# Kernel tuning notes

Hardware: AMD Instinct MI355X
Metric: run time of the kernel (lower is better)

The kernel has to match this reference:

```python
import jax, jax.numpy as jnp
import numpy as np

HIDDEN = 2048
N_EXPERTS = 8
TOP_K = 2
MOE_INTER = 1408
NORM_TOPK = False  # config.norm_topk_prob


def setup_inputs() -> dict:
    key = jax.random.key(0)
    k0, k1, k2, k3, k4 = jax.random.split(key, 5)
    hidden_states = jax.random.normal(k0, (2, 2048, HIDDEN), dtype=jnp.float32)
    # router gate: nn.Linear(hidden, num_experts, bias=False) -> store as [H, E]
    gate_w = jax.random.normal(k1, (HIDDEN, N_EXPERTS), dtype=jnp.float32) * 0.02
    # per-expert MLP weights, stacked over experts (Linear is x @ W.T, stored pre-transposed)
    w_gate = jax.random.normal(k2, (N_EXPERTS, HIDDEN, MOE_INTER), dtype=jnp.float32) * 0.02
    w_up = jax.random.normal(k3, (N_EXPERTS, HIDDEN, MOE_INTER), dtype=jnp.float32) * 0.02
    w_down = jax.random.normal(k4, (N_EXPERTS, MOE_INTER, HIDDEN), dtype=jnp.float32) * 0.02
    return {"hidden_states": hidden_states, "gate_w": gate_w,
            "w_gate": w_gate, "w_up": w_up, "w_down": w_down}


def reference(hidden_states, gate_w, w_gate, w_up, w_down):
    B, S, H = hidden_states.shape
    x = hidden_states.reshape(-1, H)                      # [T, H]
    T = x.shape[0]
    router_logits = x @ gate_w                            # [T, E]
    probs = jax.nn.softmax(router_logits.astype(jnp.float32), axis=-1)
    routing_weights, selected = jax.lax.top_k(probs, TOP_K)  # [T, K], [T, K]
    if NORM_TOPK:
        routing_weights = routing_weights / routing_weights.sum(-1, keepdims=True)
    routing_weights = routing_weights.astype(x.dtype)
    # dense combine weights [T, E]: scatter top-k weights to expert slots
    combine = jnp.zeros((T, N_EXPERTS), dtype=x.dtype)
    combine = combine.at[jnp.arange(T)[:, None], selected].add(routing_weights)
    # run all experts densely (reference form of gather-MLP-scatter)
    g = jnp.einsum('th,ehf->tef', x, w_gate)              # [T, E, F]
    u = jnp.einsum('th,ehf->tef', x, w_up)
    h = jax.nn.silu(g) * u
    y = jnp.einsum('tef,efh->teh', h, w_down)             # [T, E, H]
    out = jnp.einsum('te,teh->th', combine, y)            # [T, H]
    return out
```

## Files before the change

kernel.cpp:

```cpp
#include <hip/hip_runtime.h>
#include <hip/hip_bf16.h>

#define HID  2048
#define NEXP 8
#define FINT 1408
#define TM   128
#define BK   32
#define GU_NP 11
#define DN_NP 8
#define MAXT 96

typedef __bf16 bf16_t;
typedef __bf16 bf16x8 __attribute__((ext_vector_type(8)));
typedef float  f32x4  __attribute__((ext_vector_type(4)));

#define AS1 __attribute__((address_space(1)))
#define AS3 __attribute__((address_space(3)))

__device__ __forceinline__ void gll16(const void* g, void* l) {
    __builtin_amdgcn_global_load_lds((const AS1 void*)g, (AS3 void*)l, 16, 0, 0);
}

#define VMCNT6() asm volatile("s_waitcnt vmcnt(6)" ::: "memory")
#define VMCNT0() asm volatile("s_waitcnt vmcnt(0)" ::: "memory")
#define SB0() __builtin_amdgcn_sched_barrier(0)

__global__ __launch_bounds__(64) void router_kernel(
    const float* __restrict__ x, const float* __restrict__ gw,
    int* __restrict__ cnt, int* __restrict__ topk_id, float* __restrict__ topk_w,
    bf16_t* __restrict__ xb, int T)
{
    int t = blockIdx.x;
    if (t >= T) return;
    int lane = threadIdx.x;
    float acc[NEXP];
#pragma unroll
    for (int e = 0; e < NEXP; ++e) acc[e] = 0.f;
    const float* xr = x + (size_t)t * HID;
    bf16_t* xo = xb + (size_t)t * HID;
    for (int i = lane; i < HID; i += 64) {
        float xv = xr[i];
        xo[i] = (bf16_t)xv;
        const float4* g4 = (const float4*)(gw + (size_t)i * NEXP);
        float4 a = g4[0], b = g4[1];
        acc[0] += xv * a.x; acc[1] += xv * a.y; acc[2] += xv * a.z; acc[3] += xv * a.w;
        acc[4] += xv * b.x; acc[5] += xv * b.y; acc[6] += xv * b.z; acc[7] += xv * b.w;
    }
#pragma unroll
    for (int d = 1; d < 64; d <<= 1) {
#pragma unroll
        for (int e = 0; e < NEXP; ++e) acc[e] += __shfl_xor(acc[e], d, 64);
    }
    float mx = acc[0];
#pragma unroll
    for (int e = 1; e < NEXP; ++e) mx = fmaxf(mx, acc[e]);
    float p[NEXP]; float s = 0.f;
#pragma unroll
    for (int e = 0; e < NEXP; ++e) { p[e] = expf(acc[e] - mx); s += p[e]; }
    float inv = 1.f / s;
    int i1 = 0;
#pragma unroll
    for (int e = 1; e < NEXP; ++e) if (acc[e] > acc[i1]) i1 = e;
    int i2 = (i1 == 0) ? 1 : 0;
#pragma unroll
    for (int e = 0; e < NEXP; ++e) if (e != i1 && acc[e] > acc[i2]) i2 = e;
    if (lane == 0) {
        topk_id[t * 2 + 0] = i1; topk_id[t * 2 + 1] = i2;
        topk_w[t * 2 + 0] = p[i1] * inv; topk_w[t * 2 + 1] = p[i2] * inv;
        atomicAdd(&cnt[i1], 1); atomicAdd(&cnt[i2], 1);
    }
}

__global__ void offsets_kernel(const int* __restrict__ cnt, int* __restrict__ offs,
                               int* __restrict__ tile_e, int* __restrict__ tile_r,
                               int* __restrict__ ntl)
{
    if (threadIdx.x == 0) {
        int s = 0;
        for (int e = 0; e < NEXP; ++e) { offs[e] = s; s += cnt[e]; }
        offs[NEXP] = s;
        int k = 0;
        for (int e = 0; e < NEXP; ++e)
            for (int rb = 0; rb < cnt[e] && k < MAXT; rb += TM) { tile_e[k] = e; tile_r[k] = rb; ++k; }
        ntl[0] = k;
    }
}

__global__ void scatter_kernel(
    const int* __restrict__ topk_id, const int* __restrict__ offs, int* __restrict__ fill,
    int* __restrict__ tok, int* __restrict__ slot_of, int T)
{
    int t = blockIdx.x * blockDim.x + threadIdx.x;
    if (t >= T) return;
#pragma unroll
    for (int k = 0; k < 2; ++k) {
        int e = topk_id[t * 2 + k];
        int pos = atomicAdd(&fill[e], 1);
        int slot = offs[e] + pos;
        tok[slot] = t;
        slot_of[t * 2 + k] = slot;
    }
}

__global__ __launch_bounds__(256) void cvt_t_kernel(
    const float* __restrict__ in, bf16_t* __restrict__ outb, int R, int C)
{
    int tilesR = R >> 6, tilesC = C >> 6;
    int per = tilesR * tilesC;
    int e = blockIdx.x / per;
    int rem = blockIdx.x - e * per;
    int tr = rem / tilesC, tc = rem - tr * tilesC;
    const float* src = in + (size_t)e * R * C + (size_t)(tr * 64) * C + tc * 64;
    bf16_t* dst = outb + (size_t)e * R * C + (size_t)(tc * 64) * R + tr * 64;

    __shared__ float tile[64][65];
    int tid = threadIdx.x;
    int rr = tid >> 4;
    int cc = (tid & 15) * 4;
#pragma unroll
    for (int i = 0; i < 4; ++i) {
        float4 v = *(const float4*)(src + (size_t)(rr + i * 16) * C + cc);
        tile[rr + i * 16][cc + 0] = v.x; tile[rr + i * 16][cc + 1] = v.y;
        tile[rr + i * 16][cc + 2] = v.z; tile[rr + i * 16][cc + 3] = v.w;
    }
    __syncthreads();
    int oc = tid >> 2;
    int og = (tid & 3) * 16;
    bf16_t* dp = dst + (size_t)oc * R + og;
    bf16x8 o0, o1;
#pragma unroll
    for (int j = 0; j < 8; ++j) { o0[j] = (bf16_t)tile[og + j][oc]; o1[j] = (bf16_t)tile[og + 8 + j][oc]; }
    *(bf16x8*)dp = o0;
    *(bf16x8*)(dp + 8) = o1;
}

__global__ __launch_bounds__(256, 2) void gateup3_kernel(
    const bf16_t* __restrict__ xb, const bf16_t* __restrict__ wgb, const bf16_t* __restrict__ wub,
    const int* __restrict__ offs, const int* __restrict__ tok,
    const int* __restrict__ tile_e, const int* __restrict__ tile_r, const int* __restrict__ ntl,
    bf16_t* __restrict__ h_buf)
{
    __shared__ bf16_t smem[36864];
    const int ntiles = ntl[0];
    const int nitems = ntiles * GU_NP;
    const int tid = threadIdx.x;
    const int lane = tid & 63, w = tid >> 6;
    const int lr = lane & 15, lg = lane >> 4;
    const int rl = lane >> 2;
    const int sw8 = ((lane & 3) ^ ((lane >> 3) & 3)) * 8;
    const int ksw = (lg ^ ((lr >> 1) & 3)) * 8;

    for (int item = blockIdx.x; item < nitems; item += (int)gridDim.x) {
        const int ti = item / GU_NP;
        const int fp = item - ti * GU_NP;
        const int e = tile_e[ti], rbase = tile_r[ti];
        const int seg0 = offs[e];
        const int nvalid = min(offs[e + 1] - seg0 - rbase, TM);
        const int row0 = seg0 + rbase;
        const int f0 = fp * 128;

        const bf16_t* aP[2];
#pragma unroll
        for (int i = 0; i < 2; ++i) {
            int r = w * 32 + i * 16 + rl;
            int tk = tok[row0 + min(r, nvalid - 1)];
            aP[i] = xb + (size_t)tk * HID + sw8;
        }
        const bf16_t* bP[4];
#pragma unroll
        for (int j = 0; j < 4; ++j) {
            int br = w * 64 + j * 16 + rl;
            const bf16_t* W = (br < 128) ? wgb : wub;
            bP[j] = W + ((size_t)e * FINT + f0 + (br & 127)) * HID + sw8;
        }

        f32x4 acc[8][4];
#pragma unroll
        for (int mi = 0; mi < 8; ++mi)
#pragma unroll
            for (int ni = 0; ni < 4; ++ni) acc[mi][ni] = (f32x4){0.f, 0.f, 0.f, 0.f};

        auto STAGE = [&](int b, int kt) {
            int k0 = kt * BK;
            bf16_t* A = smem + b * 4096;
            bf16_t* B = smem + 12288 + b * 8192;
            gll16(aP[0] + k0, A + (w * 2 + 0) * 512);
            gll16(aP[1] + k0, A + (w * 2 + 1) * 512);
            gll16(bP[0] + k0, B + (w * 4 + 0) * 512);
            gll16(bP[1] + k0, B + (w * 4 + 1) * 512);
            gll16(bP[2] + k0, B + (w * 4 + 2) * 512);
            gll16(bP[3] + k0, B + (w * 4 + 3) * 512);
        };
        auto COMPUTE = [&](int b) {
            const bf16_t* A = smem + b * 4096;
            const bf16_t* B = smem + 12288 + b * 8192;
            bf16x8 bfr[4];
#pragma unroll
            for (int ni = 0; ni < 4; ++ni)
                bfr[ni] = *(const bf16x8*)&B[(w * 64 + ni * 16 + lr) * BK + ksw];
#pragma unroll
            for (int mi = 0; mi < 8; ++mi) {
                bf16x8 a = *(const bf16x8*)&A[(mi * 16 + lr) * BK + ksw];
#pragma unroll
                for (int ni = 0; ni < 4; ++ni)
                    acc[mi][ni] = __builtin_amdgcn_mfma_f32_16x16x32_bf16(a, bfr[ni], acc[mi][ni], 0, 0, 0);
            }
        };

        const int NK = HID / BK;
        STAGE(0, 0); STAGE(1, 1);
        int c0 = 0, c1 = 1, c2 = 2;
        for (int kt = 0; kt < NK - 1; ++kt) {
            SB0(); VMCNT6(); __builtin_amdgcn_s_barrier(); SB0();
            if (kt + 2 < NK) STAGE(c2, kt + 2);
            SB0();
            COMPUTE(c0);
            int t = c0; c0 = c1; c1 = c2; c2 = t;
        }
        SB0(); VMCNT0(); __builtin_amdgcn_s_barrier(); SB0();
        COMPUTE(c0);
        __syncthreads();

        if (w >= 2) {
#pragma unroll
            for (int mi = 0; mi < 8; ++mi)
#pragma unroll
                for (int ni = 0; ni < 4; ++ni)
#pragma unroll
                    for (int rr = 0; rr < 4; ++rr) {
                        int row = mi * 16 + lg * 4 + rr;
                        int col = (w - 2) * 64 + ni * 16 + lr;
                        smem[row * 128 + col] = (bf16_t)acc[mi][ni][rr];
                    }
        }
        __syncthreads();
        if (w < 2) {
#pragma unroll
            for (int mi = 0; mi < 8; ++mi)
#pragma unroll
                for (int ni = 0; ni < 4; ++ni)
#pragma unroll
                    for (int rr = 0; rr < 4; ++rr) {
                        int row = mi * 16 + lg * 4 + rr;
                        int col = w * 64 + ni * 16 + lr;
                        float g = acc[mi][ni][rr];
                        float u = (float)smem[row * 128 + col];
                        float h = (g / (1.f + __expf(-g))) * u;
                        if (row < nvalid)
                            h_buf[(size_t)(row0 + row) * FINT + f0 + col] = (bf16_t)h;
                    }
        }
        __syncthreads();
    }
}

__global__ __launch_bounds__(256, 2) void down3_kernel(
    const bf16_t* __restrict__ h_buf, const bf16_t* __restrict__ wdb,
    const int* __restrict__ offs, const int* __restrict__ tile_e, const int* __restrict__ tile_r,
    const int* __restrict__ ntl, bf16_t* __restrict__ y_buf)
{
    __shared__ bf16_t smem[36864];
    const int ntiles = ntl[0];
    const int nitems = ntiles * DN_NP;
    const int tid = threadIdx.x;
    const int lane = tid & 63, w = tid >> 6;
    const int lr = lane & 15, lg = lane >> 4;
    const int rl = lane >> 2;
    const int sw8 = ((lane & 3) ^ ((lane >> 3) & 3)) * 8;
    const int ksw = (lg ^ ((lr >> 1) & 3)) * 8;

    for (int item = blockIdx.x; item < nitems; item += (int)gridDim.x) {
        const int ti = item / DN_NP;
        const int hp = item - ti * DN_NP;
        const int e = tile_e[ti], rbase = tile_r[ti];
        const int seg0 = offs[e];
        const int nvalid = min(offs[e + 1] - seg0 - rbase, TM);
        const int row0 = seg0 + rbase;
        const int h0 = hp * 256;

        const bf16_t* aP[2];
#pragma unroll
        for (int i = 0; i < 2; ++i) {
            int r = w * 32 + i * 16 + rl;
            aP[i] = h_buf + (size_t)(row0 + r) * FINT + sw8;
        }
        const bf16_t* bP[4];
#pragma unroll
        for (int j = 0; j < 4; ++j) {
            int br = w * 64 + j * 16 + rl;
            bP[j] = wdb + ((size_t)e * HID + h0 + br) * FINT + sw8;
        }

        f32x4 acc[8][4];
#pragma unroll
        for (int mi = 0; mi < 8; ++mi)
#pragma unroll
            for (int ni = 0; ni < 4; ++ni) acc[mi][ni] = (f32x4){0.f, 0.f, 0.f, 0.f};

        auto STAGE = [&](int b, int kt) {
            int k0 = kt * BK;
            bf16_t* A = smem + b * 4096;
            bf16_t* B = smem + 12288 + b * 8192;
            gll16(aP[0] + k0, A + (w * 2 + 0) * 512);
            gll16(aP[1] + k0, A + (w * 2 + 1) * 512);
            gll16(bP[0] + k0, B + (w * 4 + 0) * 512);
            gll16(bP[1] + k0, B + (w * 4 + 1) * 512);
            gll16(bP[2] + k0, B + (w * 4 + 2) * 512);
            gll16(bP[3] + k0, B + (w * 4 + 3) * 512);
        };
        auto COMPUTE = [&](int b) {
            const bf16_t* A = smem + b * 4096;
            const bf16_t* B = smem + 12288 + b * 8192;
            bf16x8 bfr[4];
#pragma unroll
            for (int ni = 0; ni < 4; ++ni)
                bfr[ni] = *(const bf16x8*)&B[(w * 64 + ni * 16 + lr) * BK + ksw];
#pragma unroll
            for (int mi = 0; mi < 8; ++mi) {
                bf16x8 a = *(const bf16x8*)&A[(mi * 16 + lr) * BK + ksw];
#pragma unroll
                for (int ni = 0; ni < 4; ++ni)
                    acc[mi][ni] = __builtin_amdgcn_mfma_f32_16x16x32_bf16(a, bfr[ni], acc[mi][ni], 0, 0, 0);
            }
        };

        const int NK = FINT / BK;
        STAGE(0, 0); STAGE(1, 1);
        int c0 = 0, c1 = 1, c2 = 2;
        for (int kt = 0; kt < NK - 1; ++kt) {
            SB0(); VMCNT6(); __builtin_amdgcn_s_barrier(); SB0();
            if (kt + 2 < NK) STAGE(c2, kt + 2);
            SB0();
            COMPUTE(c0);
            int t = c0; c0 = c1; c1 = c2; c2 = t;
        }
        SB0(); VMCNT0(); __builtin_amdgcn_s_barrier(); SB0();
        COMPUTE(c0);

#pragma unroll
        for (int mi = 0; mi < 8; ++mi)
#pragma unroll
            for (int ni = 0; ni < 4; ++ni)
#pragma unroll
                for (int rr = 0; rr < 4; ++rr) {
                    int row = mi * 16 + lg * 4 + rr;
                    int col = w * 64 + ni * 16 + lr;
                    if (row < nvalid)
                        y_buf[(size_t)(row0 + row) * HID + h0 + col] = (bf16_t)acc[mi][ni][rr];
                }
        __syncthreads();
    }
}

__global__ __launch_bounds__(256) void combine_kernel(
    const bf16_t* __restrict__ y, const int* __restrict__ slot_of,
    const float* __restrict__ topk_w, float* __restrict__ out, int T)
{
    int t = blockIdx.x;
    int tid = threadIdx.x;
    int s0 = slot_of[t * 2], s1 = slot_of[t * 2 + 1];
    float w0 = topk_w[t * 2], w1 = topk_w[t * 2 + 1];
    const bf16x8* y0 = (const bf16x8*)(y + (size_t)s0 * HID);
    const bf16x8* y1 = (const bf16x8*)(y + (size_t)s1 * HID);
    bf16x8 v0 = y0[tid], v1 = y1[tid];
    float* op = out + (size_t)t * HID + tid * 8;
#pragma unroll
    for (int j = 0; j < 8; ++j)
        op[j] = w0 * (float)v0[j] + w1 * (float)v1[j];
}

extern "C" void kernel_launch(void* const* d_in, const int* in_sizes, int n_in,
                              void* d_out, int out_size, void* d_ws, size_t ws_size,
                              hipStream_t stream)
{
    const float* x  = (const float*)d_in[0];
    const float* gw = (const float*)d_in[1];
    const float* wg = (const float*)d_in[2];
    const float* wu = (const float*)d_in[3];
    const float* wd = (const float*)d_in[4];
    float* out = (float*)d_out;
    int T = in_sizes[0] / HID;
    int S2 = 2 * T;

    char* base = (char*)d_ws;
    int* cnt     = (int*)base;
    int* fill    = cnt + 8;
    int* offs    = cnt + 16;
    int* ntl     = cnt + 28;
    int* tile_e  = cnt + 32;
    int* tile_r  = cnt + 128;
    int* topk_id = cnt + 224;
    float* topk_w = (float*)(topk_id + S2);
    int* tok     = (int*)(topk_w + S2);
    int* slot_of = tok + S2 + 256;
    size_t small_end = (size_t)((char*)(slot_of + S2) - base);
    size_t cur = (small_end + 255) & ~(size_t)255;
    auto take = [&](size_t bytes) -> size_t {
        size_t o = cur; cur += bytes; cur = (cur + 255) & ~(size_t)255; return o;
    };
    size_t wbytes = (size_t)NEXP * HID * FINT * 2;
    size_t o_xb  = take((size_t)T * HID * 2);
    size_t o_wgb = take(wbytes);
    size_t o_wub = take(wbytes);
    size_t o_wdb = take(wbytes);
    size_t o_h   = take((size_t)(S2 + 256) * FINT * 2);
    size_t o_y   = take((size_t)(S2 + 256) * HID * 2);
    (void)ws_size;

    bf16_t* xb   = (bf16_t*)(base + o_xb);
    bf16_t* wgb  = (bf16_t*)(base + o_wgb);
    bf16_t* wub  = (bf16_t*)(base + o_wub);
    bf16_t* wdb  = (bf16_t*)(base + o_wdb);
    bf16_t* h_buf = (bf16_t*)(base + o_h);
    bf16_t* y_buf = (bf16_t*)(base + o_y);

    hipMemsetAsync(base, 0, 64, stream);

    router_kernel<<<T, 64, 0, stream>>>(x, gw, cnt, topk_id, topk_w, xb, T);
    offsets_kernel<<<1, 64, 0, stream>>>(cnt, offs, tile_e, tile_r, ntl);
    scatter_kernel<<<(T + 255) / 256, 256, 0, stream>>>(topk_id, offs, fill, tok, slot_of, T);

    int gridW = NEXP * (HID / 64) * (FINT / 64);
    cvt_t_kernel<<<gridW, 256, 0, stream>>>(wg, wgb, HID, FINT);
    cvt_t_kernel<<<gridW, 256, 0, stream>>>(wu, wub, HID, FINT);
    cvt_t_kernel<<<gridW, 256, 0, stream>>>(wd, wdb, FINT, HID);

    gateup3_kernel<<<512, 256, 0, stream>>>(xb, wgb, wub, offs, tok, tile_e, tile_r, ntl, h_buf);
    down3_kernel<<<512, 256, 0, stream>>>(h_buf, wdb, offs, tile_e, tile_r, ntl, y_buf);
    combine_kernel<<<T, 256, 0, stream>>>(y_buf, slot_of, topk_w, out, T);
}
```

Baseline: 504.5 us.

## Use 256-row tiles with 512-thread blocks and XCD-aware weight-panel scheduling

Doubles the M tile to 256 token rows and moves the expert GEMMs to 512-thread blocks with a 4x2 wave layout, so each weight panel is loaded once for twice as many tokens. The offsets kernel now builds per-XCD work lists that group items by weight panel (expert, column panel), so blocks on the same XCD share panels in L2. It also folds the pipeline epilogue into the main loop. The cost is more LDS per block (96KB) and coarser load balance, since there are fewer, larger work items.

```diff
diff --git a/kernel.cpp b/kernel.cpp
--- a/kernel.cpp
+++ b/kernel.cpp
@@ -4,11 +4,10 @@
 #define HID  2048
 #define NEXP 8
 #define FINT 1408
-#define TM   128
+#define TM   256
 #define BK   32
-#define GU_NP 11
-#define DN_NP 8
-#define MAXT 96
+#define GU_NPAN 88
+#define DN_NPAN 64
 
 typedef __bf16 bf16_t;
 typedef __bf16 bf16x8 __attribute__((ext_vector_type(8)));
@@ -21,7 +20,7 @@
     __builtin_amdgcn_global_load_lds((const AS1 void*)g, (AS3 void*)l, 16, 0, 0);
 }
 
-#define VMCNT6() asm volatile("s_waitcnt vmcnt(6)" ::: "memory")
+#define VMCNT4() asm volatile("s_waitcnt vmcnt(4)" ::: "memory")
 #define VMCNT0() asm volatile("s_waitcnt vmcnt(0)" ::: "memory")
 #define SB0() __builtin_amdgcn_sched_barrier(0)
 
@@ -72,17 +71,34 @@
 }
 
 __global__ void offsets_kernel(const int* __restrict__ cnt, int* __restrict__ offs,
-                               int* __restrict__ tile_e, int* __restrict__ tile_r,
-                               int* __restrict__ ntl)
+                               int* __restrict__ gbase, int* __restrict__ gcount,
+                               int* __restrict__ dbase, int* __restrict__ dcount,
+                               int* __restrict__ gu, int* __restrict__ dn)
 {
     if (threadIdx.x == 0) {
         int s = 0;
         for (int e = 0; e < NEXP; ++e) { offs[e] = s; s += cnt[e]; }
         offs[NEXP] = s;
         int k = 0;
-        for (int e = 0; e < NEXP; ++e)
-            for (int rb = 0; rb < cnt[e] && k < MAXT; rb += TM) { tile_e[k] = e; tile_r[k] = rb; ++k; }
-        ntl[0] = k;
+        for (int x = 0; x < 8; ++x) {
+            gbase[x] = k;
+            for (int p = x; p < GU_NPAN; p += 8) {
+                int e = p / 11, fp = p - e * 11;
+                int nt = (cnt[e] + TM - 1) / TM;
+                for (int t = 0; t < nt; ++t) gu[k++] = (e << 10) | (fp << 6) | t;
+            }
+            gcount[x] = k - gbase[x];
+        }
+        k = 0;
+        for (int x = 0; x < 8; ++x) {
+            dbase[x] = k;
+            for (int p = x; p < DN_NPAN; p += 8) {
+                int e = p >> 3, hp = p & 7;
+                int nt = (cnt[e] + TM - 1) / TM;
+                for (int t = 0; t < nt; ++t) dn[k++] = (e << 10) | (hp << 6) | t;
+            }
+            dcount[x] = k - dbase[x];
+        }
     }
 }
 
@@ -134,27 +150,29 @@
     *(bf16x8*)(dp + 8) = o1;
 }
 
-__global__ __launch_bounds__(256, 2) void gateup3_kernel(
+__global__ __launch_bounds__(512, 2) void gateup3_kernel(
     const bf16_t* __restrict__ xb, const bf16_t* __restrict__ wgb, const bf16_t* __restrict__ wub,
     const int* __restrict__ offs, const int* __restrict__ tok,
-    const int* __restrict__ tile_e, const int* __restrict__ tile_r, const int* __restrict__ ntl,
+    const int* __restrict__ gbase, const int* __restrict__ gcount, const int* __restrict__ gu,
     bf16_t* __restrict__ h_buf)
 {
-    __shared__ bf16_t smem[36864];
-    const int ntiles = ntl[0];
-    const int nitems = ntiles * GU_NP;
+    __shared__ bf16_t smem[49152];
     const int tid = threadIdx.x;
     const int lane = tid & 63, w = tid >> 6;
+    const int wm = w >> 1, wn = w & 1;
     const int lr = lane & 15, lg = lane >> 4;
     const int rl = lane >> 2;
     const int sw8 = ((lane & 3) ^ ((lane >> 3) & 3)) * 8;
     const int ksw = (lg ^ ((lr >> 1) & 3)) * 8;
 
-    for (int item = blockIdx.x; item < nitems; item += (int)gridDim.x) {
-        const int ti = item / GU_NP;
-        const int fp = item - ti * GU_NP;
-        const int e = tile_e[ti], rbase = tile_r[ti];
+    const int xcd = blockIdx.x & 7, slot = blockIdx.x >> 3;
+    const int icnt = gcount[xcd], ib = gbase[xcd];
+
+    for (int ii = slot; ii < icnt; ii += 32) {
+        const int it = gu[ib + ii];
+        const int e = it >> 10, fp = (it >> 6) & 15, tr = it & 63;
         const int seg0 = offs[e];
+        const int rbase = tr * TM;
         const int nvalid = min(offs[e + 1] - seg0 - rbase, TM);
         const int row0 = seg0 + rbase;
         const int f0 = fp * 128;
@@ -162,47 +180,45 @@
         const bf16_t* aP[2];
 #pragma unroll
         for (int i = 0; i < 2; ++i) {
-            int r = w * 32 + i * 16 + rl;
+            int r = (w * 2 + i) * 16 + rl;
             int tk = tok[row0 + min(r, nvalid - 1)];
             aP[i] = xb + (size_t)tk * HID + sw8;
         }
-        const bf16_t* bP[4];
-#pragma unroll
-        for (int j = 0; j < 4; ++j) {
-            int br = w * 64 + j * 16 + rl;
+        const bf16_t* bP[2];
+#pragma unroll
+        for (int i = 0; i < 2; ++i) {
+            int br = (w * 2 + i) * 16 + rl;
             const bf16_t* W = (br < 128) ? wgb : wub;
-            bP[j] = W + ((size_t)e * FINT + f0 + (br & 127)) * HID + sw8;
-        }
-
-        f32x4 acc[8][4];
-#pragma unroll
-        for (int mi = 0; mi < 8; ++mi)
-#pragma unroll
-            for (int ni = 0; ni < 4; ++ni) acc[mi][ni] = (f32x4){0.f, 0.f, 0.f, 0.f};
+            bP[i] = W + ((size_t)e * FINT + f0 + (br & 127)) * HID + sw8;
+        }
+
+        f32x4 acc[4][8];
+#pragma unroll
+        for (int mi = 0; mi < 4; ++mi)
+#pragma unroll
+            for (int ni = 0; ni < 8; ++ni) acc[mi][ni] = (f32x4){0.f, 0.f, 0.f, 0.f};
 
         auto STAGE = [&](int b, int kt) {
             int k0 = kt * BK;
-            bf16_t* A = smem + b * 4096;
-            bf16_t* B = smem + 12288 + b * 8192;
+            bf16_t* A = smem + b * 8192;
+            bf16_t* B = smem + 24576 + b * 8192;
             gll16(aP[0] + k0, A + (w * 2 + 0) * 512);
             gll16(aP[1] + k0, A + (w * 2 + 1) * 512);
-            gll16(bP[0] + k0, B + (w * 4 + 0) * 512);
-            gll16(bP[1] + k0, B + (w * 4 + 1) * 512);
-            gll16(bP[2] + k0, B + (w * 4 + 2) * 512);
-            gll16(bP[3] + k0, B + (w * 4 + 3) * 512);
+            gll16(bP[0] + k0, B + (w * 2 + 0) * 512);
+            gll16(bP[1] + k0, B + (w * 2 + 1) * 512);
         };
         auto COMPUTE = [&](int b) {
-            const bf16_t* A = smem + b * 4096;
-            const bf16_t* B = smem + 12288 + b * 8192;
-            bf16x8 bfr[4];
-#pragma unroll
-            for (int ni = 0; ni < 4; ++ni)
-                bfr[ni] = *(const bf16x8*)&B[(w * 64 + ni * 16 + lr) * BK + ksw];
-#pragma unroll
-            for (int mi = 0; mi < 8; ++mi) {
-                bf16x8 a = *(const bf16x8*)&A[(mi * 16 + lr) * BK + ksw];
-#pragma unroll
-                for (int ni = 0; ni < 4; ++ni)
+            const bf16_t* A = smem + b * 8192;
+            const bf16_t* B = smem + 24576 + b * 8192;
+            bf16x8 bfr[8];
+#pragma unroll
+            for (int ni = 0; ni < 8; ++ni)
+                bfr[ni] = *(const bf16x8*)&B[(wn * 128 + ni * 16 + lr) * BK + ksw];
+#pragma unroll
+            for (int mi = 0; mi < 4; ++mi) {
+                bf16x8 a = *(const bf16x8*)&A[(wm * 64 + mi * 16 + lr) * BK + ksw];
+#pragma unroll
+                for (int ni = 0; ni < 8; ++ni)
                     acc[mi][ni] = __builtin_amdgcn_mfma_f32_16x16x32_bf16(a, bfr[ni], acc[mi][ni], 0, 0, 0);
             }
         };
@@ -210,39 +226,40 @@
         const int NK = HID / BK;
         STAGE(0, 0); STAGE(1, 1);
         int c0 = 0, c1 = 1, c2 = 2;
-        for (int kt = 0; kt < NK - 1; ++kt) {
-            SB0(); VMCNT6(); __builtin_amdgcn_s_barrier(); SB0();
+        for (int kt = 0; kt < NK; ++kt) {
+            SB0();
+            if (kt + 1 < NK) { VMCNT4(); } else { VMCNT0(); }
+            __builtin_amdgcn_s_barrier();
+            SB0();
             if (kt + 2 < NK) STAGE(c2, kt + 2);
             SB0();
             COMPUTE(c0);
             int t = c0; c0 = c1; c1 = c2; c2 = t;
         }
-        SB0(); VMCNT0(); __builtin_amdgcn_s_barrier(); SB0();
-        COMPUTE(c0);
         __syncthreads();
 
-        if (w >= 2) {
-#pragma unroll
-            for (int mi = 0; mi < 8; ++mi)
-#pragma unroll
-                for (int ni = 0; ni < 4; ++ni)
+        if (wn == 1) {
+#pragma unroll
+            for (int mi = 0; mi < 4; ++mi)
+#pragma unroll
+                for (int ni = 0; ni < 8; ++ni)
 #pragma unroll
                     for (int rr = 0; rr < 4; ++rr) {
-                        int row = mi * 16 + lg * 4 + rr;
-                        int col = (w - 2) * 64 + ni * 16 + lr;
+                        int row = wm * 64 + mi * 16 + lg * 4 + rr;
+                        int col = ni * 16 + lr;
                         smem[row * 128 + col] = (bf16_t)acc[mi][ni][rr];
                     }
         }
         __syncthreads();
-        if (w < 2) {
-#pragma unroll
-            for (int mi = 0; mi < 8; ++mi)
-#pragma unroll
-                for (int ni = 0; ni < 4; ++ni)
+        if (wn == 0) {
+#pragma unroll
+            for (int mi = 0; mi < 4; ++mi)
+#pragma unroll
+                for (int ni = 0; ni < 8; ++ni)
 #pragma unroll
                     for (int rr = 0; rr < 4; ++rr) {
-                        int row = mi * 16 + lg * 4 + rr;
-                        int col = w * 64 + ni * 16 + lr;
+                        int row = wm * 64 + mi * 16 + lg * 4 + rr;
+                        int col = ni * 16 + lr;
                         float g = acc[mi][ni][rr];
                         float u = (float)smem[row * 128 + col];
                         float h = (g / (1.f + __expf(-g))) * u;
@@ -254,26 +271,29 @@
     }
 }
 
-__global__ __launch_bounds__(256, 2) void down3_kernel(
+__global__ __launch_bounds__(512, 2) void down3_kernel(
     const bf16_t* __restrict__ h_buf, const bf16_t* __restrict__ wdb,
-    const int* __restrict__ offs, const int* __restrict__ tile_e, const int* __restrict__ tile_r,
-    const int* __restrict__ ntl, bf16_t* __restrict__ y_buf)
-{
-    __shared__ bf16_t smem[36864];
-    const int ntiles = ntl[0];
-    const int nitems = ntiles * DN_NP;
+    const int* __restrict__ offs,
+    const int* __restrict__ dbase, const int* __restrict__ dcount, const int* __restrict__ dn,
+    bf16_t* __restrict__ y_buf)
+{
+    __shared__ bf16_t smem[49152];
     const int tid = threadIdx.x;
     const int lane = tid & 63, w = tid >> 6;
+    const int wm = w >> 1, wn = w & 1;
     const int lr = lane & 15, lg = lane >> 4;
     const int rl = lane >> 2;
     const int sw8 = ((lane & 3) ^ ((lane >> 3) & 3)) * 8;
     const int ksw = (lg ^ ((lr >> 1) & 3)) * 8;
 
-    for (int item = blockIdx.x; item < nitems; item += (int)gridDim.x) {
-        const int ti = item / DN_NP;
-        const int hp = item - ti * DN_NP;
-        const int e = tile_e[ti], rbase = tile_r[ti];
+    const int xcd = blockIdx.x & 7, slot = blockIdx.x >> 3;
+    const int icnt = dcount[xcd], ib = dbase[xcd];
+
+    for (int ii = slot; ii < icnt; ii += 32) {
+        const int it = dn[ib + ii];
+        const int e = it >> 10, hp = (it >> 6) & 15, tr = it & 63;
         const int seg0 = offs[e];
+        const int rbase = tr * TM;
         const int nvalid = min(offs[e + 1] - seg0 - rbase, TM);
         const int row0 = seg0 + rbase;
         const int h0 = hp * 256;
@@ -281,45 +301,43 @@
         const bf16_t* aP[2];
 #pragma unroll
         for (int i = 0; i < 2; ++i) {
-            int r = w * 32 + i * 16 + rl;
+            int r = (w * 2 + i) * 16 + rl;
             aP[i] = h_buf + (size_t)(row0 + r) * FINT + sw8;
         }
-        const bf16_t* bP[4];
-#pragma unroll
-        for (int j = 0; j < 4; ++j) {
-            int br = w * 64 + j * 16 + rl;
-            bP[j] = wdb + ((size_t)e * HID + h0 + br) * FINT + sw8;
-        }
-
-        f32x4 acc[8][4];
-#pragma unroll
-        for (int mi = 0; mi < 8; ++mi)
-#pragma unroll
-            for (int ni = 0; ni < 4; ++ni) acc[mi][ni] = (f32x4){0.f, 0.f, 0.f, 0.f};
+        const bf16_t* bP[2];
+#pragma unroll
+        for (int i = 0; i < 2; ++i) {
+            int br = (w * 2 + i) * 16 + rl;
+            bP[i] = wdb + ((size_t)e * HID + h0 + br) * FINT + sw8;
+        }
+
+        f32x4 acc[4][8];
+#pragma unroll
+        for (int mi = 0; mi < 4; ++mi)
+#pragma unroll
+            for (int ni = 0; ni < 8; ++ni) acc[mi][ni] = (f32x4){0.f, 0.f, 0.f, 0.f};
 
         auto STAGE = [&](int b, int kt) {
             int k0 = kt * BK;
-            bf16_t* A = smem + b * 4096;
-            bf16_t* B = smem + 12288 + b * 8192;
+            bf16_t* A = smem + b * 8192;
+            bf16_t* B = smem + 24576 + b * 8192;
             gll16(aP[0] + k0, A + (w * 2 + 0) * 512);
             gll16(aP[1] + k0, A + (w * 2 + 1) * 512);
-            gll16(bP[0] + k0, B + (w * 4 + 0) * 512);
-            gll16(bP[1] + k0, B + (w * 4 + 1) * 512);
-            gll16(bP[2] + k0, B + (w * 4 + 2) * 512);
-            gll16(bP[3] + k0, B + (w * 4 + 3) * 512);
+            gll16(bP[0] + k0, B + (w * 2 + 0) * 512);
+            gll16(bP[1] + k0, B + (w * 2 + 1) * 512);
         };
         auto COMPUTE = [&](int b) {
-            const bf16_t* A = smem + b * 4096;
-            const bf16_t* B = smem + 12288 + b * 8192;
-            bf16x8 bfr[4];
-#pragma unroll
-            for (int ni = 0; ni < 4; ++ni)
-                bfr[ni] = *(const bf16x8*)&B[(w * 64 + ni * 16 + lr) * BK + ksw];
-#pragma unroll
-            for (int mi = 0; mi < 8; ++mi) {
-                bf16x8 a = *(const bf16x8*)&A[(mi * 16 + lr) * BK + ksw];
-#pragma unroll
-                for (int ni = 0; ni < 4; ++ni)
+            const bf16_t* A = smem + b * 8192;
+            const bf16_t* B = smem + 24576 + b * 8192;
+            bf16x8 bfr[8];
+#pragma unroll
+            for (int ni = 0; ni < 8; ++ni)
+                bfr[ni] = *(const bf16x8*)&B[(wn * 128 + ni * 16 + lr) * BK + ksw];
+#pragma unroll
+            for (int mi = 0; mi < 4; ++mi) {
+                bf16x8 a = *(const bf16x8*)&A[(wm * 64 + mi * 16 + lr) * BK + ksw];
+#pragma unroll
+                for (int ni = 0; ni < 8; ++ni)
                     acc[mi][ni] = __builtin_amdgcn_mfma_f32_16x16x32_bf16(a, bfr[ni], acc[mi][ni], 0, 0, 0);
             }
         };
@@ -327,24 +345,25 @@
         const int NK = FINT / BK;
         STAGE(0, 0); STAGE(1, 1);
         int c0 = 0, c1 = 1, c2 = 2;
-        for (int kt = 0; kt < NK - 1; ++kt) {
-            SB0(); VMCNT6(); __builtin_amdgcn_s_barrier(); SB0();
+        for (int kt = 0; kt < NK; ++kt) {
+            SB0();
+            if (kt + 1 < NK) { VMCNT4(); } else { VMCNT0(); }
+            __builtin_amdgcn_s_barrier();
+            SB0();
             if (kt + 2 < NK) STAGE(c2, kt + 2);
             SB0();
             COMPUTE(c0);
             int t = c0; c0 = c1; c1 = c2; c2 = t;
         }
-        SB0(); VMCNT0(); __builtin_amdgcn_s_barrier(); SB0();
-        COMPUTE(c0);
-
-#pragma unroll
-        for (int mi = 0; mi < 8; ++mi)
-#pragma unroll
-            for (int ni = 0; ni < 4; ++ni)
+
+#pragma unroll
+        for (int mi = 0; mi < 4; ++mi)
+#pragma unroll
+            for (int ni = 0; ni < 8; ++ni)
 #pragma unroll
                 for (int rr = 0; rr < 4; ++rr) {
-                    int row = mi * 16 + lg * 4 + rr;
-                    int col = w * 64 + ni * 16 + lr;
+                    int row = wm * 64 + mi * 16 + lg * 4 + rr;
+                    int col = wn * 128 + ni * 16 + lr;
                     if (row < nvalid)
                         y_buf[(size_t)(row0 + row) * HID + h0 + col] = (bf16_t)acc[mi][ni][rr];
                 }
@@ -386,10 +405,13 @@
     int* cnt     = (int*)base;
     int* fill    = cnt + 8;
     int* offs    = cnt + 16;
-    int* ntl     = cnt + 28;
-    int* tile_e  = cnt + 32;
-    int* tile_r  = cnt + 128;
-    int* topk_id = cnt + 224;
+    int* gbase   = cnt + 32;
+    int* gcount  = cnt + 40;
+    int* dbase   = cnt + 48;
+    int* dcount  = cnt + 56;
+    int* gu      = cnt + 64;
+    int* dnl     = cnt + 576;
+    int* topk_id = cnt + 960;
     float* topk_w = (float*)(topk_id + S2);
     int* tok     = (int*)(topk_w + S2);
     int* slot_of = tok + S2 + 256;
@@ -407,17 +429,17 @@
     size_t o_y   = take((size_t)(S2 + 256) * HID * 2);
     (void)ws_size;
 
-    bf16_t* xb   = (bf16_t*)(base + o_xb);
-    bf16_t* wgb  = (bf16_t*)(base + o_wgb);
-    bf16_t* wub  = (bf16_t*)(base + o_wub);
-    bf16_t* wdb  = (bf16_t*)(base + o_wdb);
+    bf16_t* xb    = (bf16_t*)(base + o_xb);
+    bf16_t* wgb   = (bf16_t*)(base + o_wgb);
+    bf16_t* wub   = (bf16_t*)(base + o_wub);
+    bf16_t* wdb   = (bf16_t*)(base + o_wdb);
     bf16_t* h_buf = (bf16_t*)(base + o_h);
     bf16_t* y_buf = (bf16_t*)(base + o_y);
 
     hipMemsetAsync(base, 0, 64, stream);
 
     router_kernel<<<T, 64, 0, stream>>>(x, gw, cnt, topk_id, topk_w, xb, T);
-    offsets_kernel<<<1, 64, 0, stream>>>(cnt, offs, tile_e, tile_r, ntl);
+    offsets_kernel<<<1, 64, 0, stream>>>(cnt, offs, gbase, gcount, dbase, dcount, gu, dnl);
     scatter_kernel<<<(T + 255) / 256, 256, 0, stream>>>(topk_id, offs, fill, tok, slot_of, T);
 
     int gridW = NEXP * (HID / 64) * (FINT / 64);
@@ -425,7 +447,7 @@
     cvt_t_kernel<<<gridW, 256, 0, stream>>>(wu, wub, HID, FINT);
     cvt_t_kernel<<<gridW, 256, 0, stream>>>(wd, wdb, FINT, HID);
 
-    gateup3_kernel<<<512, 256, 0, stream>>>(xb, wgb, wub, offs, tok, tile_e, tile_r, ntl, h_buf);
-    down3_kernel<<<512, 256, 0, stream>>>(h_buf, wdb, offs, tile_e, tile_r, ntl, y_buf);
+    gateup3_kernel<<<256, 512, 0, stream>>>(xb, wgb, wub, offs, tok, gbase, gcount, gu, h_buf);
+    down3_kernel<<<256, 512, 0, stream>>>(h_buf, wdb, offs, dbase, dcount, dnl, y_buf);
     combine_kernel<<<T, 256, 0, stream>>>(y_buf, slot_of, topk_w, out, T);
 }
```

Result: faster. 493.4 us (-2.2%).

## Schedule expert GEMM work items per XCD for L2 weight reuse

Applied to the files above, without the earlier changes.

Builds per-XCD work lists in the offsets kernel, assigning each weight panel (expert, column block) to one XCD so that all row tiles sharing a weight panel run on the same XCD's L2. Grids grow to 768 blocks with 96 slots per XCD. The three weight-conversion launches are merged into one, and the router loads x as float4. This adds scheduling logic and can cause load imbalance across XCDs when expert counts are skewed.

```diff
diff --git a/kernel.cpp b/kernel.cpp
--- a/kernel.cpp
+++ b/kernel.cpp
@@ -6,9 +6,8 @@
 #define FINT 1408
 #define TM   128
 #define BK   32
-#define GU_NP 11
-#define DN_NP 8
-#define MAXT 96
+#define GU_NPAN 88
+#define DN_NPAN 64
 
 typedef __bf16 bf16_t;
 typedef __bf16 bf16x8 __attribute__((ext_vector_type(8)));
@@ -38,13 +37,18 @@
     for (int e = 0; e < NEXP; ++e) acc[e] = 0.f;
     const float* xr = x + (size_t)t * HID;
     bf16_t* xo = xb + (size_t)t * HID;
-    for (int i = lane; i < HID; i += 64) {
-        float xv = xr[i];
-        xo[i] = (bf16_t)xv;
-        const float4* g4 = (const float4*)(gw + (size_t)i * NEXP);
-        float4 a = g4[0], b = g4[1];
-        acc[0] += xv * a.x; acc[1] += xv * a.y; acc[2] += xv * a.z; acc[3] += xv * a.w;
-        acc[4] += xv * b.x; acc[5] += xv * b.y; acc[6] += xv * b.z; acc[7] += xv * b.w;
+    for (int i0 = lane * 4; i0 < HID; i0 += 256) {
+        float4 xv = *(const float4*)(xr + i0);
+        bf16_t b4[4] = {(bf16_t)xv.x, (bf16_t)xv.y, (bf16_t)xv.z, (bf16_t)xv.w};
+        *(uint2*)(xo + i0) = *(uint2*)b4;
+        float xs[4] = {xv.x, xv.y, xv.z, xv.w};
+#pragma unroll
+        for (int u = 0; u < 4; ++u) {
+            const float4* g4 = (const float4*)(gw + (size_t)(i0 + u) * NEXP);
+            float4 a = g4[0], b = g4[1];
+            acc[0] += xs[u] * a.x; acc[1] += xs[u] * a.y; acc[2] += xs[u] * a.z; acc[3] += xs[u] * a.w;
+            acc[4] += xs[u] * b.x; acc[5] += xs[u] * b.y; acc[6] += xs[u] * b.z; acc[7] += xs[u] * b.w;
+        }
     }
 #pragma unroll
     for (int d = 1; d < 64; d <<= 1) {
@@ -72,17 +76,48 @@
 }
 
 __global__ void offsets_kernel(const int* __restrict__ cnt, int* __restrict__ offs,
-                               int* __restrict__ tile_e, int* __restrict__ tile_r,
-                               int* __restrict__ ntl)
-{
-    if (threadIdx.x == 0) {
+                               int* __restrict__ gbase, int* __restrict__ gcount,
+                               int* __restrict__ dbase, int* __restrict__ dcount,
+                               int* __restrict__ gu, int* __restrict__ dn)
+{
+    __shared__ int gc[8], dc[8];
+    int tid = threadIdx.x;
+    if (tid == 0) {
         int s = 0;
         for (int e = 0; e < NEXP; ++e) { offs[e] = s; s += cnt[e]; }
         offs[NEXP] = s;
-        int k = 0;
-        for (int e = 0; e < NEXP; ++e)
-            for (int rb = 0; rb < cnt[e] && k < MAXT; rb += TM) { tile_e[k] = e; tile_r[k] = rb; ++k; }
-        ntl[0] = k;
+    }
+    if (tid < 8) {
+        int c = 0;
+        for (int p = tid; p < GU_NPAN; p += 8) { int e = p / 11; c += (cnt[e] + TM - 1) / TM; }
+        gc[tid] = c;
+    } else if (tid < 16) {
+        int x = tid - 8, c = 0;
+        for (int p = x; p < DN_NPAN; p += 8) { int e = p >> 3; c += (cnt[e] + TM - 1) / TM; }
+        dc[x] = c;
+    }
+    __syncthreads();
+    if (tid < 8) {
+        int base = 0;
+        for (int i = 0; i < tid; ++i) base += gc[i];
+        gbase[tid] = base; gcount[tid] = gc[tid];
+        int k = base;
+        for (int p = tid; p < GU_NPAN; p += 8) {
+            int e = p / 11, fp = p - e * 11;
+            int nt = (cnt[e] + TM - 1) / TM;
+            for (int t = 0; t < nt; ++t) gu[k++] = (e << 10) | (fp << 6) | t;
+        }
+    } else if (tid < 16) {
+        int x = tid - 8;
+        int base = 0;
+        for (int i = 0; i < x; ++i) base += dc[i];
+        dbase[x] = base; dcount[x] = dc[x];
+        int k = base;
+        for (int p = x; p < DN_NPAN; p += 8) {
+            int e = p >> 3, hp = p & 7;
+            int nt = (cnt[e] + TM - 1) / TM;
+            for (int t = 0; t < nt; ++t) dn[k++] = (e << 10) | (hp << 6) | t;
+        }
     }
 }
 
@@ -102,13 +137,21 @@
     }
 }
 
-__global__ __launch_bounds__(256) void cvt_t_kernel(
-    const float* __restrict__ in, bf16_t* __restrict__ outb, int R, int C)
-{
-    int tilesR = R >> 6, tilesC = C >> 6;
-    int per = tilesR * tilesC;
-    int e = blockIdx.x / per;
-    int rem = blockIdx.x - e * per;
+__global__ __launch_bounds__(256) void cvt3_kernel(
+    const float* __restrict__ wg, const float* __restrict__ wu, const float* __restrict__ wd,
+    bf16_t* __restrict__ wgb, bf16_t* __restrict__ wub, bf16_t* __restrict__ wdb)
+{
+    const int per = NEXP * (HID / 64) * (FINT / 64);
+    int b = blockIdx.x;
+    const float* in; bf16_t* outb; int R, C;
+    if (b < per)            { in = wg; outb = wgb; R = HID;  C = FINT; }
+    else if (b < 2 * per)   { b -= per; in = wu; outb = wub; R = HID;  C = FINT; }
+    else                    { b -= 2 * per; in = wd; outb = wdb; R = FINT; C = HID; }
+
+    int tilesC = C >> 6;
+    int perE = (R >> 6) * tilesC;
+    int e = b / perE;
+    int rem = b - e * perE;
     int tr = rem / tilesC, tc = rem - tr * tilesC;
     const float* src = in + (size_t)e * R * C + (size_t)(tr * 64) * C + tc * 64;
     bf16_t* dst = outb + (size_t)e * R * C + (size_t)(tc * 64) * R + tr * 64;
@@ -137,12 +180,10 @@
 __global__ __launch_bounds__(256, 2) void gateup3_kernel(
     const bf16_t* __restrict__ xb, const bf16_t* __restrict__ wgb, const bf16_t* __restrict__ wub,
     const int* __restrict__ offs, const int* __restrict__ tok,
-    const int* __restrict__ tile_e, const int* __restrict__ tile_r, const int* __restrict__ ntl,
+    const int* __restrict__ gbase, const int* __restrict__ gcount, const int* __restrict__ gu,
     bf16_t* __restrict__ h_buf)
 {
     __shared__ bf16_t smem[36864];
-    const int ntiles = ntl[0];
-    const int nitems = ntiles * GU_NP;
     const int tid = threadIdx.x;
     const int lane = tid & 63, w = tid >> 6;
     const int lr = lane & 15, lg = lane >> 4;
@@ -150,11 +191,14 @@
     const int sw8 = ((lane & 3) ^ ((lane >> 3) & 3)) * 8;
     const int ksw = (lg ^ ((lr >> 1) & 3)) * 8;
 
-    for (int item = blockIdx.x; item < nitems; item += (int)gridDim.x) {
-        const int ti = item / GU_NP;
-        const int fp = item - ti * GU_NP;
-        const int e = tile_e[ti], rbase = tile_r[ti];
+    const int xcd = blockIdx.x & 7, slot = blockIdx.x >> 3;
+    const int icnt = gcount[xcd], ib = gbase[xcd];
+
+    for (int ii = slot; ii < icnt; ii += 96) {
+        const int it = gu[ib + ii];
+        const int e = it >> 10, fp = (it >> 6) & 15, tr = it & 63;
         const int seg0 = offs[e];
+        const int rbase = tr * TM;
         const int nvalid = min(offs[e + 1] - seg0 - rbase, TM);
         const int row0 = seg0 + rbase;
         const int f0 = fp * 128;
@@ -256,12 +300,11 @@
 
 __global__ __launch_bounds__(256, 2) void down3_kernel(
     const bf16_t* __restrict__ h_buf, const bf16_t* __restrict__ wdb,
-    const int* __restrict__ offs, const int* __restrict__ tile_e, const int* __restrict__ tile_r,
-    const int* __restrict__ ntl, bf16_t* __restrict__ y_buf)
+    const int* __restrict__ offs,
+    const int* __restrict__ dbase, const int* __restrict__ dcount, const int* __restrict__ dn,
+    bf16_t* __restrict__ y_buf)
 {
     __shared__ bf16_t smem[36864];
-    const int ntiles = ntl[0];
-    const int nitems = ntiles * DN_NP;
     const int tid = threadIdx.x;
     const int lane = tid & 63, w = tid >> 6;
     const int lr = lane & 15, lg = lane >> 4;
@@ -269,11 +312,14 @@
     const int sw8 = ((lane & 3) ^ ((lane >> 3) & 3)) * 8;
     const int ksw = (lg ^ ((lr >> 1) & 3)) * 8;
 
-    for (int item = blockIdx.x; item < nitems; item += (int)gridDim.x) {
-        const int ti = item / DN_NP;
-        const int hp = item - ti * DN_NP;
-        const int e = tile_e[ti], rbase = tile_r[ti];
+    const int xcd = blockIdx.x & 7, slot = blockIdx.x >> 3;
+    const int icnt = dcount[xcd], ib = dbase[xcd];
+
+    for (int ii = slot; ii < icnt; ii += 96) {
+        const int it = dn[ib + ii];
+        const int e = it >> 10, hp = (it >> 6) & 15, tr = it & 63;
         const int seg0 = offs[e];
+        const int rbase = tr * TM;
         const int nvalid = min(offs[e + 1] - seg0 - rbase, TM);
         const int row0 = seg0 + rbase;
         const int h0 = hp * 256;
@@ -282,7 +328,7 @@
 #pragma unroll
         for (int i = 0; i < 2; ++i) {
             int r = w * 32 + i * 16 + rl;
-            aP[i] = h_buf + (size_t)(row0 + r) * FINT + sw8;
+            aP[i] = h_buf + (size_t)(row0 + min(r, nvalid - 1)) * FINT + sw8;
         }
         const bf16_t* bP[4];
 #pragma unroll
@@ -386,10 +432,13 @@
     int* cnt     = (int*)base;
     int* fill    = cnt + 8;
     int* offs    = cnt + 16;
-    int* ntl     = cnt + 28;
-    int* tile_e  = cnt + 32;
-    int* tile_r  = cnt + 128;
-    int* topk_id = cnt + 224;
+    int* gbase   = cnt + 32;
+    int* gcount  = cnt + 40;
+    int* dbase   = cnt + 48;
+    int* dcount  = cnt + 56;
+    int* gu      = cnt + 64;
+    int* dnl     = cnt + 1088;
+    int* topk_id = cnt + 1856;
     float* topk_w = (float*)(topk_id + S2);
     int* tok     = (int*)(topk_w + S2);
     int* slot_of = tok + S2 + 256;
@@ -407,25 +456,23 @@
     size_t o_y   = take((size_t)(S2 + 256) * HID * 2);
     (void)ws_size;
 
-    bf16_t* xb   = (bf16_t*)(base + o_xb);
-    bf16_t* wgb  = (bf16_t*)(base + o_wgb);
-    bf16_t* wub  = (bf16_t*)(base + o_wub);
-    bf16_t* wdb  = (bf16_t*)(base + o_wdb);
+    bf16_t* xb    = (bf16_t*)(base + o_xb);
+    bf16_t* wgb   = (bf16_t*)(base + o_wgb);
+    bf16_t* wub   = (bf16_t*)(base + o_wub);
+    bf16_t* wdb   = (bf16_t*)(base + o_wdb);
     bf16_t* h_buf = (bf16_t*)(base + o_h);
     bf16_t* y_buf = (bf16_t*)(base + o_y);
 
     hipMemsetAsync(base, 0, 64, stream);
 
     router_kernel<<<T, 64, 0, stream>>>(x, gw, cnt, topk_id, topk_w, xb, T);
-    offsets_kernel<<<1, 64, 0, stream>>>(cnt, offs, tile_e, tile_r, ntl);
+    offsets_kernel<<<1, 64, 0, stream>>>(cnt, offs, gbase, gcount, dbase, dcount, gu, dnl);
     scatter_kernel<<<(T + 255) / 256, 256, 0, stream>>>(topk_id, offs, fill, tok, slot_of, T);
 
-    int gridW = NEXP * (HID / 64) * (FINT / 64);
-    cvt_t_kernel<<<gridW, 256, 0, stream>>>(wg, wgb, HID, FINT);
-    cvt_t_kernel<<<gridW, 256, 0, stream>>>(wu, wub, HID, FINT);
-    cvt_t_kernel<<<gridW, 256, 0, stream>>>(wd, wdb, FINT, HID);
-
-    gateup3_kernel<<<512, 256, 0, stream>>>(xb, wgb, wub, offs, tok, tile_e, tile_r, ntl, h_buf);
-    down3_kernel<<<512, 256, 0, stream>>>(h_buf, wdb, offs, tile_e, tile_r, ntl, y_buf);
+    int gridW = 3 * NEXP * (HID / 64) * (FINT / 64);
+    cvt3_kernel<<<gridW, 256, 0, stream>>>(wg, wu, wd, wgb, wub, wdb);
+
+    gateup3_kernel<<<768, 256, 0, stream>>>(xb, wgb, wub, offs, tok, gbase, gcount, gu, h_buf);
+    down3_kernel<<<768, 256, 0, stream>>>(h_buf, wdb, offs, dbase, dcount, dnl, y_buf);
     combine_kernel<<<T, 256, 0, stream>>>(y_buf, slot_of, topk_w, out, T);
 }
```

New measurement: 462.8 us. -8.3%, faster.
